# Kernel optimization log

Hardware: AMD Instinct MI355X
Metric: run time of the kernel (lower is better)

Reference implementation:

```python
import jax, jax.numpy as jnp
import numpy as np

KK = 10.0  # sigmoid sharpness constant `kk` from the source

def sigmoid_k(x):
    return jax.nn.sigmoid(KK * x)

def setup_inputs() -> dict:
    key = jax.random.key(0)
    k1, k2, k3 = jax.random.split(key, 3)
    B, L = 8192, 4096
    # contiguous valid-prefix padding mask with random per-row lengths in [L//4, L)
    lens = jax.random.randint(k1, (B,), L // 4, L)
    mask = (jnp.arange(L)[None, :] < lens[:, None]).astype(jnp.float32)
    t = jax.random.uniform(k2, (B, 1), dtype=jnp.float32) * L          # crop centers
    l = 1.0 + jax.random.uniform(k3, (B, 1), dtype=jnp.float32) * (L / 2.0)  # half-widths
    return {"t": t, "l": l, "mask": mask, "length": L}

def reference(t, l, mask, length):
    t = t.reshape(-1, 1)
    l = l.reshape(-1, 1)
    # boundaries of the valid region (replaces the CPU numpy argmax round-trip)
    left = (jnp.argmax(mask, axis=-1).astype(jnp.float32) - 1.0)[:, None]          # [B,1]
    right = (float(length) - jnp.argmax(mask[:, ::-1], axis=-1).astype(jnp.float32))[:, None]  # [B,1]
    sentence_length = jnp.sum(mask, axis=-1, keepdims=True) / 2.0                   # [B,1]
    l_eff = jnp.where(l <= sentence_length, sentence_length, l)
    t_left = (t - l_eff) * (t - l_eff >= left).astype(jnp.float32)
    t_left = jnp.where(t_left == 0.0, left, t_left)
    t_right = ((t + l_eff) <= right).astype(jnp.float32) * (t + l_eff)
    t_right = jnp.where(t_right == 0.0, right, t_right)
    pos = jnp.arange(length, dtype=jnp.float32)                                     # [L]
    crop_mask = sigmoid_k(pos - t_left) - sigmoid_k(pos - t_right)                  # [B,L]
    crop_mask = (crop_mask >= 0.5).astype(jnp.float32) * mask
    return crop_mask
```

## Files before the change

kernel.cpp:

```cpp
#include <hip/hip_runtime.h>
#include <hip/hip_bf16.h>
#include <climits>


#define BLOCK 256

__device__ __forceinline__ float sigmoid10(float x) {
    return 1.0f / (1.0f + expf(-10.0f * x));
}
__device__ __forceinline__ float fdiff(float p, float tl, float tr) {
    return sigmoid10(p - tl) - sigmoid10(p - tr);
}

__global__ __launch_bounds__(BLOCK) void probe_kernel(
    const float* __restrict__ t, const float* __restrict__ l,
    const float* __restrict__ mask, int2* __restrict__ ws, int B, int Llen) {
    const int row = blockIdx.x * BLOCK + threadIdx.x;
    if (row >= B) return;
    const float* mrow = mask + (size_t)row * Llen;

    int blo = -1, bhi = Llen;
    #pragma unroll 1
    for (int it = 0; it < 13; ++it) {
        int mid = (blo + bhi) >> 1;
        mid = max(mid, 0);
        const float v = mrow[mid];
        if (v > 0.5f) blo = mid; else bhi = mid;
    }
    const int len = bhi;

    int lo = 1, hi = 0;
    if (len > 0) {
        const float leftf  = -1.0f;
        const float rightf = (float)len;
        const float sl = 0.5f * (float)len;
        const float tv = t[row], lv = l[row];
        const float leff = (lv <= sl) ? sl : lv;
        float tl0 = tv - leff;
        float t_left = (tl0 >= leftf) ? tl0 : 0.0f;
        if (t_left == 0.0f) t_left = leftf;
        float tr0 = tv + leff;
        float t_right = (tr0 <= rightf) ? tr0 : 0.0f;
        if (t_right == 0.0f) t_right = rightf;

        const float c = expf(-10.0f * (t_right - t_left));
        const float b = 1.0f - 3.0f * c;
        const float disc = b * b - 4.0f * c;
        if (b > 0.0f && disc >= 0.0f) {
            const float xp = 0.5f * (b + sqrtf(disc));
            const float p_lo = t_left - 0.1f * logf(xp);
            const float p_hi = (t_left + t_right) - p_lo;
            lo = (int)ceilf(p_lo);
            hi = (int)floorf(p_hi);
            #pragma unroll 1
            for (int k = 0; k < 4 && fdiff((float)(lo - 1), t_left, t_right) >= 0.5f; ++k) --lo;
            #pragma unroll 1
            for (int k = 0; k < 4 && fdiff((float)lo, t_left, t_right) < 0.5f; ++k) ++lo;
            #pragma unroll 1
            for (int k = 0; k < 4 && fdiff((float)(hi + 1), t_left, t_right) >= 0.5f; ++k) ++hi;
            #pragma unroll 1
            for (int k = 0; k < 4 && fdiff((float)hi, t_left, t_right) < 0.5f; ++k) --hi;
        }
        lo = max(lo, 0);
        hi = min(hi, len - 1);
    }
    ws[row] = make_int2(lo, hi);
}

__global__ __launch_bounds__(BLOCK) void emit_kernel(
    const int2* __restrict__ ws, float* __restrict__ out,
    int B, int Llen, int total_waves) {
    const int lane = threadIdx.x & 63;
    const int wave0 = blockIdx.x * (BLOCK / 64) + (threadIdx.x >> 6);
    const int nvec = Llen >> 2;

    for (int row = wave0; row < B; row += total_waves) {
        const int urow = __builtin_amdgcn_readfirstlane(row);
        const int2 bnd = ws[urow];
        const int lo = bnd.x, hi = bnd.y;

        float4* orow = (float4*)(out + (size_t)urow * Llen);
        for (int j = lane; j < nvec; j += 64) {
            const int e = j << 2;
            float4 o;
            o.x = (e     >= lo && e     <= hi) ? 1.0f : 0.0f;
            o.y = (e + 1 >= lo && e + 1 <= hi) ? 1.0f : 0.0f;
            o.z = (e + 2 >= lo && e + 2 <= hi) ? 1.0f : 0.0f;
            o.w = (e + 3 >= lo && e + 3 <= hi) ? 1.0f : 0.0f;
            orow[j] = o;
        }
    }
}

extern "C" void kernel_launch(void* const* d_in, const int* in_sizes, int n_in,
                              void* d_out, int out_size, void* d_ws, size_t ws_size,
                              hipStream_t stream) {
    const float* t    = (const float*)d_in[0];
    const float* l    = (const float*)d_in[1];
    const float* mask = (const float*)d_in[2];
    float* out = (float*)d_out;
    int2* ws = (int2*)d_ws;

    const int B = in_sizes[0];
    const int Llen = in_sizes[2] / B;

    probe_kernel<<<(B + BLOCK - 1) / BLOCK, BLOCK, 0, stream>>>(t, l, mask, ws, B, Llen);

    const int blocks = 1024;
    const int total_waves = blocks * (BLOCK / 64);
    emit_kernel<<<blocks, BLOCK, 0, stream>>>(ws, out, B, Llen, total_waves);
}
```

Before: 220.1 us.

## Emit crop mask with nontemporal stores, segment loops, and whole-block rows

The emit kernel now gives each block a fixed group of rows and has all 256 threads write each row, instead of one wave per row in a grid-stride loop. Each row is split into a leading zero region, a ones region and a trailing zero region that are written with constant vectors, and only the two boundary float4s are computed per element. All stores use nontemporal hints to reduce cache pollution on the 128MB write stream. The kernel is bound by store bandwidth, so the gain depends mostly on the nontemporal stores and on the change in grid shape.

```diff
diff --git a/kernel.cpp b/kernel.cpp
--- a/kernel.cpp
+++ b/kernel.cpp
@@ -4,6 +4,8 @@
 
 
 #define BLOCK 256
+
+typedef float nfloat4 __attribute__((ext_vector_type(4)));
 
 __device__ __forceinline__ float sigmoid10(float x) {
     return 1.0f / (1.0f + expf(-10.0f * x));
@@ -68,26 +70,43 @@
 }
 
 __global__ __launch_bounds__(BLOCK) void emit_kernel(
-    const int2* __restrict__ ws, float* __restrict__ out,
-    int B, int Llen, int total_waves) {
-    const int lane = threadIdx.x & 63;
-    const int wave0 = blockIdx.x * (BLOCK / 64) + (threadIdx.x >> 6);
-    const int nvec = Llen >> 2;
+    const int2* __restrict__ ws, nfloat4* __restrict__ out,
+    int nv, int rows_per_block, int B) {
+    const int tid = threadIdx.x;
+    const int row0 = blockIdx.x * rows_per_block;
+    const nfloat4 Z = {0.0f, 0.0f, 0.0f, 0.0f};
+    const nfloat4 O = {1.0f, 1.0f, 1.0f, 1.0f};
 
-    for (int row = wave0; row < B; row += total_waves) {
-        const int urow = __builtin_amdgcn_readfirstlane(row);
-        const int2 bnd = ws[urow];
+    for (int r = 0; r < rows_per_block; ++r) {
+        const int row = row0 + r;
+        if (row >= B) return;
+        const int2 bnd = ws[row];
         const int lo = bnd.x, hi = bnd.y;
+        nfloat4* orow = out + (size_t)row * nv;
 
-        float4* orow = (float4*)(out + (size_t)urow * Llen);
-        for (int j = lane; j < nvec; j += 64) {
-            const int e = j << 2;
-            float4 o;
-            o.x = (e     >= lo && e     <= hi) ? 1.0f : 0.0f;
-            o.y = (e + 1 >= lo && e + 1 <= hi) ? 1.0f : 0.0f;
-            o.z = (e + 2 >= lo && e + 2 <= hi) ? 1.0f : 0.0f;
-            o.w = (e + 3 >= lo && e + 3 <= hi) ? 1.0f : 0.0f;
-            orow[j] = o;
+        if (lo > hi) {
+            for (int j = tid; j < nv; j += BLOCK)
+                __builtin_nontemporal_store(Z, &orow[j]);
+            continue;
+        }
+        const int qA = lo >> 2, qB = hi >> 2;
+        for (int j = tid; j < qA; j += BLOCK)
+            __builtin_nontemporal_store(Z, &orow[j]);
+        for (int j = qB + 1 + tid; j < nv; j += BLOCK)
+            __builtin_nontemporal_store(Z, &orow[j]);
+        for (int j = qA + 1 + tid; j < qB; j += BLOCK)
+            __builtin_nontemporal_store(O, &orow[j]);
+        if (tid < 2) {
+            const int q = (tid == 0) ? qA : qB;
+            if (tid == 0 || qB != qA) {
+                const int e = q << 2;
+                nfloat4 o;
+                o.x = (e     >= lo && e     <= hi) ? 1.0f : 0.0f;
+                o.y = (e + 1 >= lo && e + 1 <= hi) ? 1.0f : 0.0f;
+                o.z = (e + 2 >= lo && e + 2 <= hi) ? 1.0f : 0.0f;
+                o.w = (e + 3 >= lo && e + 3 <= hi) ? 1.0f : 0.0f;
+                __builtin_nontemporal_store(o, &orow[q]);
+            }
         }
     }
 }
@@ -106,7 +125,8 @@
 
     probe_kernel<<<(B + BLOCK - 1) / BLOCK, BLOCK, 0, stream>>>(t, l, mask, ws, B, Llen);
 
-    const int blocks = 1024;
-    const int total_waves = blocks * (BLOCK / 64);
-    emit_kernel<<<blocks, BLOCK, 0, stream>>>(ws, out, B, Llen, total_waves);
+    const int nv = Llen >> 2;
+    const int rows_per_block = 4;
+    const int blocks = (B + rows_per_block - 1) / rows_per_block;
+    emit_kernel<<<blocks, BLOCK, 0, stream>>>(ws, (nfloat4*)out, nv, rows_per_block, B);
 }
```

Result: slower. 229.4 us (+4.2%).
